# Optimization experiments

Measured on AMD Instinct MI355X. Metric: run time of the kernel, lower is better.

## Reference

```python
import jax, jax.numpy as jnp
import numpy as np

B, N = 128, 1024

def setup_inputs() -> dict:
    key = jax.random.key(0)
    k1, k2, k3 = jax.random.split(key, 3)
    m = jax.random.normal(k1, (B, N), dtype=jnp.float32)
    k = jax.random.normal(k2, (B, N, N), dtype=jnp.float32)
    targets = jax.random.randint(k3, (B,), 0, N, dtype=jnp.int64)
    return {"m": m, "k": k, "targets": targets}

def reference(m, k, targets):
    # cross_entropy: logsumexp(m) - m[targets]
    ce = jax.nn.logsumexp(m, axis=-1) - jnp.take_along_axis(m, targets[:, None], axis=-1)[:, 0]
    p = jax.nn.softmax(m, axis=-1)  # [B, N]
    # (k * (diag_embed(p) - outer(p))).sum((-2,-1))
    #   = sum_n k[b,n,n] * p[b,n]  -  p^T K p   (avoids materializing hess)
    diag_k = jnp.einsum('bnn->bn', k)                 # [B, N]
    diag_term = jnp.sum(diag_k * p, axis=-1)          # [B]
    quad_term = jnp.einsum('bn,bnm,bm->b', p, k, p)   # [B]
    return ce + 0.5 * (diag_term - quad_term)
```

## Files before the change

kernel.cpp:

```cpp
#include <hip/hip_runtime.h>

#define BB   128
#define NN   1024
#define RPB  16
#define ROWS (NN / RPB)

typedef float f4 __attribute__((ext_vector_type(4)));

__global__ __launch_bounds__(256) void fused_quad_kernel(
    const float* __restrict__ m, const float* __restrict__ k,
    const int* __restrict__ targets,
    float* __restrict__ ce, float* __restrict__ partial)
{
    const int blk = blockIdx.x;
    const int b   = blk >> 4;
    const int rb  = blk & (RPB - 1);
    const int tid = threadIdx.x;

    __shared__ float sp[NN];
    __shared__ float sred[4];

    const float* mb = m + (size_t)b * NN;
    float4 v = reinterpret_cast<const float4*>(mb)[tid];

    float mx = fmaxf(fmaxf(v.x, v.y), fmaxf(v.z, v.w));
    #pragma unroll
    for (int off = 32; off > 0; off >>= 1) mx = fmaxf(mx, __shfl_down(mx, off));
    if ((tid & 63) == 0) sred[tid >> 6] = mx;
    __syncthreads();
    mx = fmaxf(fmaxf(sred[0], sred[1]), fmaxf(sred[2], sred[3]));
    __syncthreads();

    float e0 = expf(v.x - mx), e1 = expf(v.y - mx);
    float e2 = expf(v.z - mx), e3 = expf(v.w - mx);
    float s = (e0 + e1) + (e2 + e3);
    #pragma unroll
    for (int off = 32; off > 0; off >>= 1) s += __shfl_down(s, off);
    if ((tid & 63) == 0) sred[tid >> 6] = s;
    __syncthreads();
    s = (sred[0] + sred[1]) + (sred[2] + sred[3]);

    const float inv = 1.0f / s;
    const float pm0 = e0 * inv, pm1 = e1 * inv, pm2 = e2 * inv, pm3 = e3 * inv;
    reinterpret_cast<float4*>(sp)[tid] = make_float4(pm0, pm1, pm2, pm3);
    __syncthreads();

    if (rb == 0 && tid == 0)
        ce[b] = mx + logf(s) - mb[targets[b]];

    const int m0 = 4 * tid;
    const int n0 = rb * ROWS;
    const f4* kp = reinterpret_cast<const f4*>(k + ((size_t)b * NN + n0) * NN) + tid;

    float acc = 0.0f;
    #pragma unroll 8
    for (int i = 0; i < ROWS; ++i) {
        const int n = n0 + i;
        f4    k4 = __builtin_nontemporal_load(kp + (size_t)i * (NN / 4));
        float pn = sp[n];
        float d0 = (n == m0    ) ? 1.0f : 0.0f;
        float d1 = (n == m0 + 1) ? 1.0f : 0.0f;
        float d2 = (n == m0 + 2) ? 1.0f : 0.0f;
        float d3 = (n == m0 + 3) ? 1.0f : 0.0f;
        acc += pn * (k4.x * (d0 - pm0) + k4.y * (d1 - pm1) +
                     k4.z * (d2 - pm2) + k4.w * (d3 - pm3));
    }

    #pragma unroll
    for (int off = 32; off > 0; off >>= 1) acc += __shfl_down(acc, off);
    __syncthreads();
    if ((tid & 63) == 0) sred[tid >> 6] = acc;
    __syncthreads();
    if (tid == 0) partial[blk] = (sred[0] + sred[1]) + (sred[2] + sred[3]);
}

__global__ void finalize_kernel(const float* __restrict__ ce,
                                const float* __restrict__ partial,
                                float* __restrict__ out)
{
    const int b = threadIdx.x;
    if (b < BB) {
        float s = 0.0f;
        #pragma unroll
        for (int r = 0; r < RPB; ++r) s += partial[b * RPB + r];
        out[b] = ce[b] + 0.5f * s;
    }
}

extern "C" void kernel_launch(void* const* d_in, const int* in_sizes, int n_in,
                              void* d_out, int out_size, void* d_ws, size_t ws_size,
                              hipStream_t stream)
{
    const float* m       = (const float*)d_in[0];
    const float* k       = (const float*)d_in[1];
    const int*   targets = (const int*)d_in[2];
    float*       out     = (float*)d_out;

    float* ce      = (float*)d_ws;
    float* partial = ce + BB;

    fused_quad_kernel<<<BB * RPB, 256, 0, stream>>>(m, k, targets, ce, partial);
    finalize_kernel<<<1, 128, 0, stream>>>(ce, partial, out);
}
```

Baseline: 85.22 us.

## Fuse finalize into main kernel via atomic counter and prefetch K rows early

Removes the separate finalize kernel: each block publishes its partial sum, atomically increments a per-batch counter, and the last-arriving block reduces the partials and writes the output. It also issues the first eight K row loads before the softmax reductions so memory latency overlaps the max/sum work. In exchange it adds a memset launch to reset counters and more registers for the prefetch buffer.

```diff
diff --git a/kernel.cpp b/kernel.cpp
--- a/kernel.cpp
+++ b/kernel.cpp
@@ -4,13 +4,15 @@
 #define NN   1024
 #define RPB  16
 #define ROWS (NN / RPB)
+#define PF   8
 
 typedef float f4 __attribute__((ext_vector_type(4)));
 
-__global__ __launch_bounds__(256) void fused_quad_kernel(
+__global__ __launch_bounds__(256) void fused_all_kernel(
     const float* __restrict__ m, const float* __restrict__ k,
     const int* __restrict__ targets,
-    float* __restrict__ ce, float* __restrict__ partial)
+    float* __restrict__ ce, float* __restrict__ partial,
+    unsigned int* __restrict__ cnt, float* __restrict__ out)
 {
     const int blk = blockIdx.x;
     const int b   = blk >> 4;
@@ -22,6 +24,13 @@
 
     const float* mb = m + (size_t)b * NN;
     float4 v = reinterpret_cast<const float4*>(mb)[tid];
+
+    const int n0 = rb * ROWS;
+    const f4* kp = reinterpret_cast<const f4*>(k + ((size_t)b * NN + n0) * NN) + tid;
+    f4 kpre[PF];
+    #pragma unroll
+    for (int j = 0; j < PF; ++j)
+        kpre[j] = __builtin_nontemporal_load(kp + (size_t)j * (NN / 4));
 
     float mx = fmaxf(fmaxf(v.x, v.y), fmaxf(v.z, v.w));
     #pragma unroll
@@ -46,15 +55,26 @@
     __syncthreads();
 
     if (rb == 0 && tid == 0)
-        ce[b] = mx + logf(s) - mb[targets[b]];
+        __hip_atomic_store(&ce[b], mx + logf(s) - mb[targets[b]],
+                           __ATOMIC_RELAXED, __HIP_MEMORY_SCOPE_AGENT);
 
     const int m0 = 4 * tid;
-    const int n0 = rb * ROWS;
-    const f4* kp = reinterpret_cast<const f4*>(k + ((size_t)b * NN + n0) * NN) + tid;
+    float acc = 0.0f;
+    #pragma unroll
+    for (int j = 0; j < PF; ++j) {
+        const int n = n0 + j;
+        f4    k4 = kpre[j];
+        float pn = sp[n];
+        float d0 = (n == m0    ) ? 1.0f : 0.0f;
+        float d1 = (n == m0 + 1) ? 1.0f : 0.0f;
+        float d2 = (n == m0 + 2) ? 1.0f : 0.0f;
+        float d3 = (n == m0 + 3) ? 1.0f : 0.0f;
+        acc += pn * (k4.x * (d0 - pm0) + k4.y * (d1 - pm1) +
+                     k4.z * (d2 - pm2) + k4.w * (d3 - pm3));
+    }
 
-    float acc = 0.0f;
     #pragma unroll 8
-    for (int i = 0; i < ROWS; ++i) {
+    for (int i = PF; i < ROWS; ++i) {
         const int n = n0 + i;
         f4    k4 = __builtin_nontemporal_load(kp + (size_t)i * (NN / 4));
         float pn = sp[n];
@@ -71,19 +91,23 @@
     __syncthreads();
     if ((tid & 63) == 0) sred[tid >> 6] = acc;
     __syncthreads();
-    if (tid == 0) partial[blk] = (sred[0] + sred[1]) + (sred[2] + sred[3]);
-}
 
-__global__ void finalize_kernel(const float* __restrict__ ce,
-                                const float* __restrict__ partial,
-                                float* __restrict__ out)
-{
-    const int b = threadIdx.x;
-    if (b < BB) {
-        float s = 0.0f;
-        #pragma unroll
-        for (int r = 0; r < RPB; ++r) s += partial[b * RPB + r];
-        out[b] = ce[b] + 0.5f * s;
+    if (tid == 0) {
+        float bs = (sred[0] + sred[1]) + (sred[2] + sred[3]);
+        __hip_atomic_store(&partial[blk], bs,
+                           __ATOMIC_RELAXED, __HIP_MEMORY_SCOPE_AGENT);
+        unsigned old = __hip_atomic_fetch_add(&cnt[b], 1u,
+                           __ATOMIC_ACQ_REL, __HIP_MEMORY_SCOPE_AGENT);
+        if (old == RPB - 1) {
+            float qsum = 0.0f;
+            #pragma unroll
+            for (int r = 0; r < RPB; ++r)
+                qsum += __hip_atomic_load(&partial[b * RPB + r],
+                           __ATOMIC_RELAXED, __HIP_MEMORY_SCOPE_AGENT);
+            float cev = __hip_atomic_load(&ce[b],
+                           __ATOMIC_RELAXED, __HIP_MEMORY_SCOPE_AGENT);
+            out[b] = cev + 0.5f * qsum;
+        }
     }
 }
 
@@ -96,9 +120,10 @@
     const int*   targets = (const int*)d_in[2];
     float*       out     = (float*)d_out;
 
-    float* ce      = (float*)d_ws;
-    float* partial = ce + BB;
+    float*        ce      = (float*)d_ws;
+    float*        partial = ce + BB;
+    unsigned int* cnt     = (unsigned int*)(partial + (size_t)BB * RPB);
 
-    fused_quad_kernel<<<BB * RPB, 256, 0, stream>>>(m, k, targets, ce, partial);
-    finalize_kernel<<<1, 128, 0, stream>>>(ce, partial, out);
+    hipMemsetAsync(cnt, 0, BB * sizeof(unsigned int), stream);
+    fused_all_kernel<<<BB * RPB, 256, 0, stream>>>(m, k, targets, ce, partial, cnt, out);
 }
```

Measured after the change: 183.5 us. 2.15x slower.
